# Kernel tuning notes

Hardware: AMD Instinct MI355X
Metric: run time of the kernel (lower is better)

Reference implementation:

```python
import jax, jax.numpy as jnp
import numpy as np

IN_SIZE, HIDDEN, N_STEPS = 512, 1024, 5
B, L = 32, 1024

def setup_inputs():
    key = jax.random.key(0)
    ks = jax.random.split(key, 11)
    s = 1.0 / np.sqrt(HIDDEN).astype(np.float32)
    u = lambda k, shape: jax.random.uniform(k, shape, jnp.float32, -s, s)
    return {
        "x": jax.random.normal(ks[0], (B, L, IN_SIZE), jnp.float32),
        "w_ih": u(ks[1], (3 * HIDDEN, IN_SIZE)),   # torch GRU weight_ih_l0 (gate order r,z,n)
        "w_hh": u(ks[2], (3 * HIDDEN, HIDDEN)),    # unused math-wise (h0=0) but kept for faithfulness
        "b_ih": u(ks[3], (3 * HIDDEN,)),
        "b_hh": u(ks[4], (3 * HIDDEN,)),
        "WH": u(ks[5], (N_STEPS, HIDDEN, HIDDEN)),
        "bH": u(ks[6], (N_STEPS, HIDDEN)),
        "WT": u(ks[7], (N_STEPS, HIDDEN, HIDDEN)),
        "bT": u(ks[8], (N_STEPS, HIDDEN)),
        "WC": u(ks[9], (N_STEPS, HIDDEN, HIDDEN)),
        "bC": u(ks[10], (N_STEPS, HIDDEN)),
    }

def reference(x, w_ih, w_hh, b_ih, b_hh, WH, bH, WT, bT, WC, bC):
    # Single-timestep GRU (seq_len==1 after view(-1, L, F)), h0 = 0.
    gi = jnp.einsum("blf,gf->blg", x, w_ih) + b_ih            # [B, L, 3H]
    i_r, i_z, i_n = jnp.split(gi, 3, axis=-1)
    b_hr, b_hz, b_hn = jnp.split(b_hh, 3)
    # w_hh @ h0 == 0; only the hidden biases survive.
    r = jax.nn.sigmoid(i_r + b_hr)
    z = jax.nn.sigmoid(i_z + b_hz)
    n = jnp.tanh(i_n + r * b_hn)
    h = (1.0 - z) * n                                          # h' = (1-z)*n + z*0
    # keep w_hh in the graph with zero contribution (faithful param set)
    h = h + 0.0 * jnp.sum(w_hh) * jnp.zeros_like(h[..., :1])

    def micro(h, params):
        wh, bh, wt, bt, wc, bc = params
        hh = jnp.tanh(jnp.einsum("blh,oh->blo", h, wh) + bh)
        t = jax.nn.sigmoid(jnp.einsum("blh,oh->blo", h, wt) + bt)
        c = jax.nn.sigmoid(jnp.einsum("blh,oh->blo", h, wc) + bc)
        return hh * t + h * (1.0 - c), None

    h, _ = jax.lax.scan(micro, h, (WH, bH, WT, bT, WC, bC))
    return h  # [B, L, HIDDEN], == torch.cat over batch items
```

## Files before the change

### kernel.cpp

```cpp
#include <hip/hip_runtime.h>
#include <math.h>

#define MROWS 32768
#define MH    16384
#define HID   1024
#define KGRU  512

typedef float          f32x4  __attribute__((ext_vector_type(4)));
typedef short          bf16x8 __attribute__((ext_vector_type(8)));
typedef unsigned short u16x4  __attribute__((ext_vector_type(4)));

__device__ __forceinline__ float sigm(float x) { return 1.0f / (1.0f + expf(-x)); }

__device__ __forceinline__ unsigned short f2bf(float f) {
    union { float f; unsigned u; } v; v.f = f;
    unsigned r = v.u + 0x7FFFu + ((v.u >> 16) & 1u);
    return (unsigned short)(r >> 16);
}

__device__ __forceinline__ void gld16(const void* g, void* l) {
    __builtin_amdgcn_global_load_lds((const __attribute__((address_space(1))) void*)g,
                                     (__attribute__((address_space(3))) void*)l, 16, 0, 0);
}

template <int K, bool IS_GRU>
__global__ __launch_bounds__(256, 2) void gemm3(
    const unsigned short* __restrict__ Abf,
    const unsigned short* __restrict__ W0,
    const float* __restrict__ b0, const float* __restrict__ b1, const float* __restrict__ b2,
    const float* __restrict__ bhh,
    float* __restrict__ outF,
    unsigned short* __restrict__ outBf)
{
    __shared__ short L[2][40 * 512];

    const int tid  = threadIdx.x;
    const int lane = tid & 63;
    const int wid  = tid >> 6;
    const int wm   = wid >> 1;
    const int wn   = wid & 1;
    const int l15  = lane & 15;
    const int l4   = lane >> 4;

    const int nwg = gridDim.x;
    const int cpx = nwg >> 3;
    const int wg  = blockIdx.x;
    const int swz = (wg & 7) * cpx + (wg >> 3);
    const int m0  = (swz >> 4) * 128;
    const int n0  = (swz & 15) * 64;

    long aoff[4];
#pragma unroll
    for (int i = 0; i < 4; i++) {
        const int ca = wid * 4 + i;
        const int f = ca >> 1, ks = ca & 1;
        aoff[i] = (long)(m0 + f * 16 + l15) * K + ks * 32 + l4 * 8;
    }
    long woff[6];
#pragma unroll
    for (int i = 0; i < 6; i++) {
        const int cw = wid * 6 + i;
        const int q = cw >> 3, nf = (cw >> 1) & 3, ks = cw & 1;
        woff[i] = (long)q * HID * K + (long)(n0 + nf * 16 + l15) * K + ks * 32 + l4 * 8;
    }

    const int gn0 = n0 + wn * 32 + l4 * 4;
    f32x4 hold[4][2];
    if constexpr (!IS_GRU) {
#pragma unroll
        for (int f = 0; f < 4; f++) {
            const long gm = m0 + wm * 64 + f * 16 + l15;
#pragma unroll
            for (int c = 0; c < 2; c++)
                hold[f][c] = *(const f32x4*)&outF[gm * HID + gn0 + c * 16];
        }
    }

    f32x4 acc[3][2][4];
#pragma unroll
    for (int q = 0; q < 3; q++)
#pragma unroll
        for (int c = 0; c < 2; c++)
#pragma unroll
            for (int f = 0; f < 4; f++) acc[q][c][f] = (f32x4)0.0f;

    auto stage = [&](short* Lw, int k0) {
#pragma unroll
        for (int i = 0; i < 4; i++) gld16(Abf + aoff[i] + k0, Lw + (wid * 4 + i) * 512);
#pragma unroll
        for (int i = 0; i < 6; i++) gld16(W0 + woff[i] + k0, Lw + (16 + wid * 6 + i) * 512);
    };
    auto compute = [&](const short* Lr) {
#pragma unroll
        for (int ks = 0; ks < 2; ks++) {
            bf16x8 ha[4], wb[3][2];
#pragma unroll
            for (int f = 0; f < 4; f++)
                ha[f] = *(const bf16x8*)&Lr[((wm * 4 + f) * 2 + ks) * 512 + lane * 8];
#pragma unroll
            for (int q = 0; q < 3; q++)
#pragma unroll
                for (int c = 0; c < 2; c++)
                    wb[q][c] = *(const bf16x8*)&Lr[(16 + q * 8 + (wn * 2 + c) * 2 + ks) * 512 + lane * 8];
#pragma unroll
            for (int q = 0; q < 3; q++)
#pragma unroll
                for (int c = 0; c < 2; c++)
#pragma unroll
                    for (int f = 0; f < 4; f++)
                        acc[q][c][f] = __builtin_amdgcn_mfma_f32_16x16x32_bf16(
                            wb[q][c], ha[f], acc[q][c][f], 0, 0, 0);
        }
    };

    constexpr int NT = K / 64;

    stage(L[0], 0);
    __syncthreads();

    for (int t = 0; t < NT; t += 2) {
        stage(L[1], (t + 1) * 64);
        compute(L[0]);
        __syncthreads();
        if (t + 2 < NT) stage(L[0], (t + 2) * 64);
        compute(L[1]);
        __syncthreads();
    }

    const int gn1 = gn0 + 16;
    f32x4 vb[3][2], vh[3][2];
    vb[0][0] = *(const f32x4*)&b0[gn0]; vb[0][1] = *(const f32x4*)&b0[gn1];
    vb[1][0] = *(const f32x4*)&b1[gn0]; vb[1][1] = *(const f32x4*)&b1[gn1];
    vb[2][0] = *(const f32x4*)&b2[gn0]; vb[2][1] = *(const f32x4*)&b2[gn1];
    if constexpr (IS_GRU) {
        vh[0][0] = *(const f32x4*)&bhh[gn0];           vh[0][1] = *(const f32x4*)&bhh[gn1];
        vh[1][0] = *(const f32x4*)&bhh[HID + gn0];     vh[1][1] = *(const f32x4*)&bhh[HID + gn1];
        vh[2][0] = *(const f32x4*)&bhh[2 * HID + gn0]; vh[2][1] = *(const f32x4*)&bhh[2 * HID + gn1];
    }

#pragma unroll
    for (int f = 0; f < 4; f++) {
        const long gm = m0 + wm * 64 + f * 16 + l15;
#pragma unroll
        for (int c = 0; c < 2; c++) {
            const int gn = c ? gn1 : gn0;
            const f32x4 g0 = acc[0][c][f], g1 = acc[1][c][f], g2 = acc[2][c][f];
            f32x4 res;
            if constexpr (IS_GRU) {
#pragma unroll
                for (int j = 0; j < 4; j++) {
                    float r = sigm(g0[j] + vb[0][c][j] + vh[0][c][j]);
                    float z = sigm(g1[j] + vb[1][c][j] + vh[1][c][j]);
                    float n = tanhf(g2[j] + vb[2][c][j] + r * vh[2][c][j]);
                    res[j] = (1.0f - z) * n;
                }
            } else {
#pragma unroll
                for (int j = 0; j < 4; j++) {
                    float hh = tanhf(g0[j] + vb[0][c][j]);
                    float tt = sigm(g1[j] + vb[1][c][j]);
                    float cc = sigm(g2[j] + vb[2][c][j]);
                    res[j] = hh * tt + hold[f][c][j] * (1.0f - cc);
                }
            }
            *(f32x4*)&outF[gm * HID + gn] = res;
            u16x4 rb;
#pragma unroll
            for (int j = 0; j < 4; j++) rb[j] = f2bf(res[j]);
            *(u16x4*)&outBf[gm * HID + gn] = rb;
        }
    }
}

__global__ void convP(const float* __restrict__ s, unsigned short* __restrict__ d, int n) {
    int i = (blockIdx.x * blockDim.x + threadIdx.x) * 4;
    const int stride = gridDim.x * blockDim.x * 4;
    for (; i < n; i += stride) {
        f32x4 v = *(const f32x4*)&s[i];
        u16x4 r;
#pragma unroll
        for (int j = 0; j < 4; j++) r[j] = f2bf(v[j]);
        *(u16x4*)&d[i] = r;
    }
}

__global__ void convS(const float* __restrict__ s, unsigned short* __restrict__ d, int n) {
    int i = (blockIdx.x * blockDim.x + threadIdx.x) * 4;
    const int stride = gridDim.x * blockDim.x * 4;
    for (; i < n; i += stride) {
        f32x4 v = *(const f32x4*)&s[i];
        u16x4 r;
#pragma unroll
        for (int j = 0; j < 4; j++) r[j] = f2bf(v[j]);
        const int di = (i >> 20) * (3 * HID * HID) + (i & (HID * HID - 1));
        *(u16x4*)&d[di] = r;
    }
}

extern "C" void kernel_launch(void* const* d_in, const int* in_sizes, int n_in,
                              void* d_out, int out_size, void* d_ws, size_t ws_size,
                              hipStream_t stream) {
    const float* x    = (const float*)d_in[0];
    const float* w_ih = (const float*)d_in[1];
    const float* b_ih = (const float*)d_in[3];
    const float* b_hh = (const float*)d_in[4];
    const float* WH   = (const float*)d_in[5];
    const float* bH   = (const float*)d_in[6];
    const float* WT   = (const float*)d_in[7];
    const float* bT   = (const float*)d_in[8];
    const float* WC   = (const float*)d_in[9];
    const float* bC   = (const float*)d_in[10];

    float* out = (float*)d_out;
    char*  ws  = (char*)d_ws;

    unsigned short* wih_bf = (unsigned short*)ws;
    unsigned short* W_bf   = (unsigned short*)(ws + (size_t)3 * HID * KGRU * 2);
    const size_t off_ping  = (size_t)3 * HID * KGRU * 2 + (size_t)15 * HID * HID * 2;
    unsigned short* ping   = (unsigned short*)(ws + off_ping);
    unsigned short* pong   = (unsigned short*)(ws + off_ping + (size_t)MH * HID * 2);

    dim3 blk(256);

    convP<<<1024, blk, 0, stream>>>(w_ih, wih_bf, 3 * HID * KGRU);
    convS<<<2048, blk, 0, stream>>>(WH, W_bf + 0 * HID * HID, 5 * HID * HID);
    convS<<<2048, blk, 0, stream>>>(WT, W_bf + 1 * HID * HID, 5 * HID * HID);
    convS<<<2048, blk, 0, stream>>>(WC, W_bf + 2 * HID * HID, 5 * HID * HID);

    for (int h = 0; h < 2; h++) {
        const float* xh   = x + (size_t)h * MH * KGRU;
        float*       outh = out + (size_t)h * MH * HID;

        convP<<<2048, blk, 0, stream>>>(xh, pong, MH * KGRU);

        gemm3<KGRU, true><<<2048, blk, 0, stream>>>(
            pong, wih_bf, b_ih, b_ih + HID, b_ih + 2 * HID, b_hh, outh, ping);

        const unsigned short* src = ping;
        for (int s = 0; s < 5; s++) {
            unsigned short* dst = (s & 1) ? ping : pong;
            gemm3<HID, false><<<2048, blk, 0, stream>>>(
                src, W_bf + (size_t)s * 3 * HID * HID,
                bH + s * HID, bT + s * HID, bC + s * HID, nullptr, outh, dst);
            src = dst;
        }
    }
}
```

Baseline: 2.254 ms.

## Enlarge GEMM tile to 256 rows with 512 threads and a waitcnt-driven multi-buffer pipeline

The fused three-gate GEMM now uses 512-thread blocks covering 256 rows by 64 columns, so each weight tile is reused by twice as many rows and half as many blocks are launched. LDS moves to dynamic allocation with A triple-buffered and W double-buffered, and __syncthreads is replaced by raw s_barrier plus explicit vmcnt waits so global-to-LDS loads for later K-tiles run while the current tile's MFMAs execute. MFMA bursts are split per gate and raised with s_setprio, and the residual load is moved after the main loop to free registers. The cost is 144 KB of LDS per block, which allows only one block per CU, plus reliance on hand-written waitcnt ordering being correct.

```diff
diff --git a/kernel.cpp b/kernel.cpp
--- a/kernel.cpp
+++ b/kernel.cpp
@@ -23,8 +23,12 @@
                                      (__attribute__((address_space(3))) void*)l, 16, 0, 0);
 }
 
+#define SBAR()   asm volatile("s_barrier" ::: "memory")
+#define VMCNT4() asm volatile("s_waitcnt vmcnt(4)" ::: "memory")
+#define VMCNT0() asm volatile("s_waitcnt vmcnt(0)" ::: "memory")
+
 template <int K, bool IS_GRU>
-__global__ __launch_bounds__(256, 2) void gemm3(
+__global__ __launch_bounds__(512, 2) void gemm3(
     const unsigned short* __restrict__ Abf,
     const unsigned short* __restrict__ W0,
     const float* __restrict__ b0, const float* __restrict__ b1, const float* __restrict__ b2,
@@ -32,7 +36,12 @@
     float* __restrict__ outF,
     unsigned short* __restrict__ outBf)
 {
-    __shared__ short L[2][40 * 512];
+    constexpr int NT = K / 64;
+    static_assert(NT >= 3, "pipeline needs >=3 K-tiles");
+
+    extern __shared__ short Lds[];
+    short* const Abase = Lds;
+    short* const Wbase = Lds + 3 * 16384;
 
     const int tid  = threadIdx.x;
     const int lane = tid & 63;
@@ -46,7 +55,7 @@
     const int cpx = nwg >> 3;
     const int wg  = blockIdx.x;
     const int swz = (wg & 7) * cpx + (wg >> 3);
-    const int m0  = (swz >> 4) * 128;
+    const int m0  = (swz >> 4) * 256;
     const int n0  = (swz & 15) * 64;
 
     long aoff[4];
@@ -56,77 +65,108 @@
         const int f = ca >> 1, ks = ca & 1;
         aoff[i] = (long)(m0 + f * 16 + l15) * K + ks * 32 + l4 * 8;
     }
-    long woff[6];
-#pragma unroll
-    for (int i = 0; i < 6; i++) {
-        const int cw = wid * 6 + i;
-        const int q = cw >> 3, nf = (cw >> 1) & 3, ks = cw & 1;
-        woff[i] = (long)q * HID * K + (long)(n0 + nf * 16 + l15) * K + ks * 32 + l4 * 8;
+    long woff[3];
+#pragma unroll
+    for (int i = 0; i < 3; i++) {
+        woff[i] = (long)i * HID * K + (long)(n0 + ((wid >> 1) & 3) * 16 + l15) * K
+                + (wid & 1) * 32 + l4 * 8;
+    }
+
+    f32x4 acc[3][2][4];
+#pragma unroll
+    for (int q = 0; q < 3; q++)
+#pragma unroll
+        for (int c = 0; c < 2; c++)
+#pragma unroll
+            for (int f = 0; f < 4; f++) acc[q][c][f] = (f32x4)0.0f;
+
+#pragma unroll
+    for (int i = 0; i < 4; i++) gld16(Abf + aoff[i],      Abase + (wid * 4 + i) * 512);
+#pragma unroll
+    for (int i = 0; i < 3; i++) gld16(W0 + woff[i],       Wbase + (wid + i * 8) * 512);
+#pragma unroll
+    for (int i = 0; i < 4; i++) gld16(Abf + aoff[i] + 64, Abase + 16384 + (wid * 4 + i) * 512);
+    VMCNT4();
+
+    for (int t = 0; t < NT; ++t) {
+        const short* At = Abase + (t % 3) * 16384;
+        const short* Wc = Wbase + (t & 1) * 12288;
+
+        SBAR();
+        bf16x8 ha[4][2], wb[2][2];
+#pragma unroll
+        for (int f = 0; f < 4; f++)
+#pragma unroll
+            for (int ks = 0; ks < 2; ks++)
+                ha[f][ks] = *(const bf16x8*)&At[((wm * 4 + f) * 2 + ks) * 512 + lane * 8];
+#pragma unroll
+        for (int c = 0; c < 2; c++)
+#pragma unroll
+            for (int ks = 0; ks < 2; ks++)
+                wb[c][ks] = *(const bf16x8*)&Wc[((wn * 2 + c) * 2 + ks) * 512 + lane * 8];
+        if (t + 1 < NT) {
+            short* Wn = Wbase + ((t + 1) & 1) * 12288;
+#pragma unroll
+            for (int i = 0; i < 3; i++)
+                gld16(W0 + woff[i] + (long)(t + 1) * 64, Wn + (wid + i * 8) * 512);
+        }
+        if (t + 2 < NT) {
+            short* An = Abase + ((t + 2) % 3) * 16384;
+#pragma unroll
+            for (int i = 0; i < 4; i++)
+                gld16(Abf + aoff[i] + (long)(t + 2) * 64, An + (wid * 4 + i) * 512);
+        }
+        __builtin_amdgcn_s_setprio(1);
+#pragma unroll
+        for (int c = 0; c < 2; c++)
+#pragma unroll
+            for (int f = 0; f < 4; f++)
+#pragma unroll
+                for (int ks = 0; ks < 2; ks++)
+                    acc[0][c][f] = __builtin_amdgcn_mfma_f32_16x16x32_bf16(
+                        wb[c][ks], ha[f][ks], acc[0][c][f], 0, 0, 0);
+        __builtin_amdgcn_s_setprio(0);
+
+        SBAR();
+#pragma unroll
+        for (int c = 0; c < 2; c++)
+#pragma unroll
+            for (int ks = 0; ks < 2; ks++)
+                wb[c][ks] = *(const bf16x8*)&Wc[(8 + (wn * 2 + c) * 2 + ks) * 512 + lane * 8];
+        __builtin_amdgcn_s_setprio(1);
+#pragma unroll
+        for (int c = 0; c < 2; c++)
+#pragma unroll
+            for (int f = 0; f < 4; f++)
+#pragma unroll
+                for (int ks = 0; ks < 2; ks++)
+                    acc[1][c][f] = __builtin_amdgcn_mfma_f32_16x16x32_bf16(
+                        wb[c][ks], ha[f][ks], acc[1][c][f], 0, 0, 0);
+        __builtin_amdgcn_s_setprio(0);
+
+        SBAR();
+#pragma unroll
+        for (int c = 0; c < 2; c++)
+#pragma unroll
+            for (int ks = 0; ks < 2; ks++)
+                wb[c][ks] = *(const bf16x8*)&Wc[(16 + (wn * 2 + c) * 2 + ks) * 512 + lane * 8];
+        __builtin_amdgcn_s_setprio(1);
+#pragma unroll
+        for (int c = 0; c < 2; c++)
+#pragma unroll
+            for (int f = 0; f < 4; f++)
+#pragma unroll
+                for (int ks = 0; ks < 2; ks++)
+                    acc[2][c][f] = __builtin_amdgcn_mfma_f32_16x16x32_bf16(
+                        wb[c][ks], ha[f][ks], acc[2][c][f], 0, 0, 0);
+        __builtin_amdgcn_s_setprio(0);
+
+        __builtin_amdgcn_sched_barrier(0);
+        if (t < NT - 2)       { VMCNT4(); }
+        else if (t == NT - 2) { VMCNT0(); }
     }
 
     const int gn0 = n0 + wn * 32 + l4 * 4;
-    f32x4 hold[4][2];
-    if constexpr (!IS_GRU) {
-#pragma unroll
-        for (int f = 0; f < 4; f++) {
-            const long gm = m0 + wm * 64 + f * 16 + l15;
-#pragma unroll
-            for (int c = 0; c < 2; c++)
-                hold[f][c] = *(const f32x4*)&outF[gm * HID + gn0 + c * 16];
-        }
-    }
-
-    f32x4 acc[3][2][4];
-#pragma unroll
-    for (int q = 0; q < 3; q++)
-#pragma unroll
-        for (int c = 0; c < 2; c++)
-#pragma unroll
-            for (int f = 0; f < 4; f++) acc[q][c][f] = (f32x4)0.0f;
-
-    auto stage = [&](short* Lw, int k0) {
-#pragma unroll
-        for (int i = 0; i < 4; i++) gld16(Abf + aoff[i] + k0, Lw + (wid * 4 + i) * 512);
-#pragma unroll
-        for (int i = 0; i < 6; i++) gld16(W0 + woff[i] + k0, Lw + (16 + wid * 6 + i) * 512);
-    };
-    auto compute = [&](const short* Lr) {
-#pragma unroll
-        for (int ks = 0; ks < 2; ks++) {
-            bf16x8 ha[4], wb[3][2];
-#pragma unroll
-            for (int f = 0; f < 4; f++)
-                ha[f] = *(const bf16x8*)&Lr[((wm * 4 + f) * 2 + ks) * 512 + lane * 8];
-#pragma unroll
-            for (int q = 0; q < 3; q++)
-#pragma unroll
-                for (int c = 0; c < 2; c++)
-                    wb[q][c] = *(const bf16x8*)&Lr[(16 + q * 8 + (wn * 2 + c) * 2 + ks) * 512 + lane * 8];
-#pragma unroll
-            for (int q = 0; q < 3; q++)
-#pragma unroll
-                for (int c = 0; c < 2; c++)
-#pragma unroll
-                    for (int f = 0; f < 4; f++)
-                        acc[q][c][f] = __builtin_amdgcn_mfma_f32_16x16x32_bf16(
-                            wb[q][c], ha[f], acc[q][c][f], 0, 0, 0);
-        }
-    };
-
-    constexpr int NT = K / 64;
-
-    stage(L[0], 0);
-    __syncthreads();
-
-    for (int t = 0; t < NT; t += 2) {
-        stage(L[1], (t + 1) * 64);
-        compute(L[0]);
-        __syncthreads();
-        if (t + 2 < NT) stage(L[0], (t + 2) * 64);
-        compute(L[1]);
-        __syncthreads();
-    }
-
     const int gn1 = gn0 + 16;
     f32x4 vb[3][2], vh[3][2];
     vb[0][0] = *(const f32x4*)&b0[gn0]; vb[0][1] = *(const f32x4*)&b0[gn1];
@@ -136,6 +176,16 @@
         vh[0][0] = *(const f32x4*)&bhh[gn0];           vh[0][1] = *(const f32x4*)&bhh[gn1];
         vh[1][0] = *(const f32x4*)&bhh[HID + gn0];     vh[1][1] = *(const f32x4*)&bhh[HID + gn1];
         vh[2][0] = *(const f32x4*)&bhh[2 * HID + gn0]; vh[2][1] = *(const f32x4*)&bhh[2 * HID + gn1];
+    }
+    f32x4 hold[4][2];
+    if constexpr (!IS_GRU) {
+#pragma unroll
+        for (int f = 0; f < 4; f++) {
+            const long gm = m0 + wm * 64 + f * 16 + l15;
+#pragma unroll
+            for (int c = 0; c < 2; c++)
+                hold[f][c] = *(const f32x4*)&outF[gm * HID + gn0 + c * 16];
+        }
     }
 
 #pragma unroll
@@ -220,7 +270,15 @@
     unsigned short* ping   = (unsigned short*)(ws + off_ping);
     unsigned short* pong   = (unsigned short*)(ws + off_ping + (size_t)MH * HID * 2);
 
+    const int LDS_BYTES = 147456;
+    (void)hipFuncSetAttribute((const void*)gemm3<KGRU, true>,
+                              hipFuncAttributeMaxDynamicSharedMemorySize, LDS_BYTES);
+    (void)hipFuncSetAttribute((const void*)gemm3<HID, false>,
+                              hipFuncAttributeMaxDynamicSharedMemorySize, LDS_BYTES);
+
     dim3 blk(256);
+    dim3 gblk(512);
+    dim3 ggrid(1024);
 
     convP<<<1024, blk, 0, stream>>>(w_ih, wih_bf, 3 * HID * KGRU);
     convS<<<2048, blk, 0, stream>>>(WH, W_bf + 0 * HID * HID, 5 * HID * HID);
@@ -233,13 +291,13 @@
 
         convP<<<2048, blk, 0, stream>>>(xh, pong, MH * KGRU);
 
-        gemm3<KGRU, true><<<2048, blk, 0, stream>>>(
+        gemm3<KGRU, true><<<ggrid, gblk, LDS_BYTES, stream>>>(
             pong, wih_bf, b_ih, b_ih + HID, b_ih + 2 * HID, b_hh, outh, ping);
 
         const unsigned short* src = ping;
         for (int s = 0; s < 5; s++) {
             unsigned short* dst = (s & 1) ? ping : pong;
-            gemm3<HID, false><<<2048, blk, 0, stream>>>(
+            gemm3<HID, false><<<ggrid, gblk, LDS_BYTES, stream>>>(
                 src, W_bf + (size_t)s * 3 * HID * HID,
                 bH + s * HID, bT + s * HID, bC + s * HID, nullptr, outh, dst);
             src = dst;
```

After: 1.933 ms. 1.17x faster.
